# Kernel tuning notes

Hardware: AMD Instinct MI355X
Metric: run time of the kernel (lower is better)

Reference implementation:

```python
import jax, jax.numpy as jnp
import numpy as np

N = 50000      # nodes
E = 800000     # edges per sampled adjacency
F_IN = 128     # input features
H = 256        # hidden
C = 112        # classes (ogbn-proteins)
L = 8          # num_layers
EPS = 1e-5     # BatchNorm eps


def setup_inputs() -> dict:
    key = jax.random.key(0)
    ks = jax.random.split(key, 8)
    x = jax.random.normal(ks[0], (N, F_IN), dtype=jnp.float32)
    edge1 = jax.random.randint(ks[1], (2, E), 0, N)
    edge2 = jax.random.randint(ks[2], (2, E), 0, N)
    in_W = jax.random.normal(ks[3], (F_IN, H), dtype=jnp.float32) * 0.05
    in_b = jnp.zeros((H,), jnp.float32)
    convW = jax.random.normal(ks[4], (L, H, H), dtype=jnp.float32) * 0.05
    convB = jnp.zeros((L, H), jnp.float32)
    bn_gamma = jnp.ones((L, H), jnp.float32)
    bn_beta = jnp.zeros((L, H), jnp.float32)
    out_W = jax.random.normal(ks[5], (H, C), dtype=jnp.float32) * 0.05
    out_b = jnp.zeros((C,), jnp.float32)
    layer_w = jax.random.normal(ks[6], (L,), dtype=jnp.float32)
    return dict(x=x, edge1=edge1, edge2=edge2, in_W=in_W, in_b=in_b,
                convW=convW, convB=convB, bn_gamma=bn_gamma, bn_beta=bn_beta,
                out_W=out_W, out_b=out_b, layer_w=layer_w)


def _gcn_norm(edge_index):
    # GCNConv default: add self-loops, sym-normalize D^{-1/2} A_hat D^{-1/2}.
    loops = jnp.arange(N)
    row = jnp.concatenate([edge_index[0], loops])  # source
    col = jnp.concatenate([edge_index[1], loops])  # target
    deg = jax.ops.segment_sum(jnp.ones_like(row, jnp.float32), col, num_segments=N)
    dinv = jnp.where(deg > 0, jax.lax.rsqrt(deg), 0.0)
    return row, col, dinv[row] * dinv[col]


def reference(x, edge1, edge2, in_W, in_b, convW, convB, bn_gamma, bn_beta,
              out_W, out_b, layer_w):
    adj1 = _gcn_norm(edge1)
    adj2 = _gcn_norm(edge2)
    h = x @ in_W + in_b                                  # input_fc: [N, H]
    w = jax.nn.softmax(layer_w)                          # residual layer weights
    acc = jnp.zeros_like(h)
    for i in range(L):
        row, col, norm = adj1 if i < L // 2 else adj2
        t = h @ convW[i] + convB[i]                      # GCNConv linear
        msg = t[row] * norm[:, None]                     # gather + scale  [E+N, H]
        h = jax.ops.segment_sum(msg, col, num_segments=N)  # scatter-add SpMM
        mu = h.mean(axis=0)                              # BatchNorm1d (batch stats)
        var = h.var(axis=0)
        h = (h - mu) * jax.lax.rsqrt(var + EPS) * bn_gamma[i] + bn_beta[i]
        h = jax.nn.relu(h)                               # dropout is identity in eval
        acc = acc + w[i] * h                             # weighted residual sum
    out = acc @ out_W + out_b                            # out_fc: [N, C]
    return jax.nn.log_softmax(out, axis=1)
```

## Files before the change

### kernel.cpp

```cpp
#include <hip/hip_runtime.h>
#include <math.h>

#define NN 50000
#define HH 256
#define FIN 128
#define CC 112
#define LL 8
#define EE 800000
#define EPSB 1e-5f
#define NGRP 8
#define NPG (NN / NGRP)

typedef unsigned short u16;
typedef unsigned int u32;
typedef __attribute__((ext_vector_type(8))) short bf16x8;
typedef __attribute__((ext_vector_type(4))) float f32x4;

__device__ __forceinline__ u16 f2bf(float f) {
    u32 u = __float_as_uint(f);
    u32 r = (u + 0x7FFFu + ((u >> 16) & 1u)) >> 16;
    return (u16)r;
}
__device__ __forceinline__ float bflo(u32 u) { return __uint_as_float(u << 16); }
__device__ __forceinline__ float bfhi(u32 u) { return __uint_as_float(u & 0xFFFF0000u); }
__device__ __forceinline__ float bf1(u16 u) { return __uint_as_float(((u32)u) << 16); }

__device__ __forceinline__ void gload16(const u16* g, u16* l) {
    __builtin_amdgcn_global_load_lds(
        (const __attribute__((address_space(1))) void*)g,
        (__attribute__((address_space(3))) void*)l, 16, 0, 0);
}

__global__ __launch_bounds__(256) void k_fill2(const int* __restrict__ ed1,
                                               const int* __restrict__ ed2,
                                               int* __restrict__ cur,
                                               u16* __restrict__ src1p,
                                               u16* __restrict__ src2p) {
    const int g = blockIdx.x & 7;
    const int bg = blockIdx.x >> 3;
    const int nthr = (gridDim.x >> 3) * 256;
    const int tid = bg * 256 + threadIdx.x;
    const int lo = g * NPG;

    for (int e = tid; e < EE; e += nthr) {
        int c = ed1[e + EE];
        if ((u32)(c - lo) < (u32)NPG) {
            int pos = atomicAdd(&cur[c], 1);
            src1p[(c << 6) + pos] = (u16)ed1[e];
        }
    }
    for (int e = tid; e < EE; e += nthr) {
        int c = ed2[e + EE];
        if ((u32)(c - lo) < (u32)NPG) {
            int pos = atomicAdd(&cur[NN + c], 1);
            src2p[(c << 6) + pos] = (u16)ed2[e];
        }
    }
}

__global__ void k_dinv2(const int* __restrict__ deg, float* __restrict__ dinv1,
                        float* __restrict__ dinv2, int n) {
    int v = blockIdx.x * blockDim.x + threadIdx.x;
    if (v >= 2 * n) return;
    float* d = (v < n) ? dinv1 : dinv2;
    int vv = (v < n) ? v : v - n;
    d[vv] = rsqrtf((float)(deg[v] + 1));
}

__global__ void k_wt(const float* __restrict__ W, u16* __restrict__ Wt, int K, int N) {
    __shared__ u16 sm[32][33];
    const float* Wl = W + (size_t)blockIdx.z * K * N;
    u16* Wtl = Wt + (size_t)blockIdx.z * K * N;
    int k0 = blockIdx.y * 32, n0 = blockIdx.x * 32;
    int tx = threadIdx.x, ty = threadIdx.y;
#pragma unroll
    for (int r = 0; r < 32; r += 8)
        sm[ty + r][tx] = f2bf(Wl[(size_t)(k0 + ty + r) * N + n0 + tx]);
    __syncthreads();
#pragma unroll
    for (int r = 0; r < 32; r += 8)
        Wtl[(size_t)(n0 + ty + r) * K + k0 + tx] = sm[tx][ty + r];
}

__global__ void k_outwt(const float* __restrict__ outW, const float* __restrict__ outb,
                        u16* __restrict__ outWt, float* __restrict__ obb) {
    int idx = blockIdx.x * 256 + threadIdx.x;
    if (idx >= 128 * 256) return;
    int n = idx >> 8, k = idx & 255;
    float v = (n < CC) ? outW[(size_t)k * CC + n] : 0.f;
    outWt[(size_t)n * HH + k] = f2bf(v);
    if (idx < 128) obb[idx] = (idx < CC) ? outb[idx] : 0.f;
}

__global__ void k_xcast(const float* __restrict__ x, u16* __restrict__ xb, int n4) {
    int i = blockIdx.x * blockDim.x + threadIdx.x;
    if (i >= n4) return;
    float4 v = ((const float4*)x)[i];
    ushort4 o;
    o.x = f2bf(v.x); o.y = f2bf(v.y); o.z = f2bf(v.z); o.w = f2bf(v.w);
    *(ushort4*)(xb + ((size_t)i << 2)) = o;
}

template <bool F32OUT, bool SWIZ>
__global__ __launch_bounds__(256) void k_gemm_bf16(const u16* __restrict__ A,
                                                   const u16* __restrict__ Bt,
                                                   const float* __restrict__ bias,
                                                   const float* __restrict__ rowscale,
                                                   void* __restrict__ Cout,
                                                   int M, int Nc, int K) {
    int m0, n0;
    if (SWIZ) {
        int id = blockIdx.x;
        int g = id >> 4, r = id & 15;
        int m = g * 8 + (r & 7);
        if (m * 128 >= M) return;
        m0 = m * 128;
        n0 = (r >> 3) * 128;
    } else {
        m0 = blockIdx.x * 128;
        n0 = 0;
    }
    __shared__ u16 As[128 * 32];
    __shared__ u16 Bs[128 * 32];
    const int tid = threadIdx.x;
    const int w = tid >> 6, lane = tid & 63;
    const int wr = (w >> 1) * 64, wc = (w & 1) * 64;
    const int lm = lane & 15, lq = lane >> 4;

    f32x4 acc[4][4];
#pragma unroll
    for (int i = 0; i < 4; ++i)
#pragma unroll
        for (int j = 0; j < 4; ++j) acc[i][j] = (f32x4){0.f, 0.f, 0.f, 0.f};

    const int srow = w * 16 + (lane >> 2);
    const int scol = (lane & 3) * 8;

    for (int k0 = 0; k0 < K; k0 += 32) {
        int gm = m0 + srow;        if (gm >= M) gm = M - 1;
        gload16(A + (size_t)gm * K + k0 + scol, As + (size_t)(w * 64) * 8);
        int gm2 = m0 + 64 + srow;  if (gm2 >= M) gm2 = M - 1;
        gload16(A + (size_t)gm2 * K + k0 + scol, As + (size_t)(256 + w * 64) * 8);
        gload16(Bt + (size_t)(n0 + srow) * K + k0 + scol, Bs + (size_t)(w * 64) * 8);
        gload16(Bt + (size_t)(n0 + 64 + srow) * K + k0 + scol, Bs + (size_t)(256 + w * 64) * 8);
        __syncthreads();

        bf16x8 af[4], bfr[4];
#pragma unroll
        for (int i = 0; i < 4; ++i)
            af[i] = *(const bf16x8*)(As + (wr + i * 16 + lm) * 32 + lq * 8);
#pragma unroll
        for (int j = 0; j < 4; ++j)
            bfr[j] = *(const bf16x8*)(Bs + (wc + j * 16 + lm) * 32 + lq * 8);
#pragma unroll
        for (int i = 0; i < 4; ++i)
#pragma unroll
            for (int j = 0; j < 4; ++j)
                acc[i][j] = __builtin_amdgcn_mfma_f32_16x16x32_bf16(af[i], bfr[j], acc[i][j], 0, 0, 0);
        __syncthreads();
    }

#pragma unroll
    for (int j = 0; j < 4; ++j) {
        int gc = n0 + wc + j * 16 + lm;
        float bj = (gc < Nc) ? bias[gc] : 0.f;
#pragma unroll
        for (int i = 0; i < 4; ++i) {
#pragma unroll
            for (int r = 0; r < 4; ++r) {
                int gr = m0 + wr + i * 16 + lq * 4 + r;
                if (gr < M && gc < Nc) {
                    float rs = rowscale ? rowscale[gr] : 1.0f;
                    float val = (acc[i][j][r] + bj) * rs;
                    if (F32OUT)
                        ((float*)Cout)[(size_t)gr * Nc + gc] = val;
                    else
                        ((u16*)Cout)[(size_t)gr * Nc + gc] = f2bf(val);
                }
            }
        }
    }
}

__global__ __launch_bounds__(512) void k_spmm_bf16(const u16* __restrict__ t,
                                                   const int* __restrict__ deg,
                                                   const u16* __restrict__ srcp,
                                                   const float* __restrict__ dinv,
                                                   u16* __restrict__ hpre,
                                                   float* __restrict__ bns,
                                                   float* __restrict__ bnq) {
    __shared__ float lsum[8][HH];
    __shared__ float lsq[8][HH];
    int w = threadIdx.x >> 6;
    int lane = threadIdx.x & 63;
    int c = lane << 2;
    const u16* tp = t + c;
    float4 ssum = make_float4(0.f, 0.f, 0.f, 0.f);
    float4 ssq  = make_float4(0.f, 0.f, 0.f, 0.f);
    int vbase = (blockIdx.x * 8 + w) * 2;

    for (int i = 0; i < 2; ++i) {
        int v = vbase + i;
        const u16* src = srcp + (v << 6);
        float dv = dinv[v];
        uint2 a = *(const uint2*)(tp + (size_t)v * HH);
        float4 accv;
        accv.x = bflo(a.x); accv.y = bfhi(a.x);
        accv.z = bflo(a.y); accv.w = bfhi(a.y);
        int end = deg[v];
        int j = 0;
        for (; j + 8 <= end; j += 8) {
            uint4 sp = *(const uint4*)(src + j);
            int s0 = sp.x & 0xFFFF, s1 = sp.x >> 16;
            int s2 = sp.y & 0xFFFF, s3 = sp.y >> 16;
            int s4 = sp.z & 0xFFFF, s5 = sp.z >> 16;
            int s6 = sp.w & 0xFFFF, s7 = sp.w >> 16;
            uint2 b0 = *(const uint2*)(tp + (size_t)s0 * HH);
            uint2 b1 = *(const uint2*)(tp + (size_t)s1 * HH);
            uint2 b2 = *(const uint2*)(tp + (size_t)s2 * HH);
            uint2 b3 = *(const uint2*)(tp + (size_t)s3 * HH);
            uint2 b4 = *(const uint2*)(tp + (size_t)s4 * HH);
            uint2 b5 = *(const uint2*)(tp + (size_t)s5 * HH);
            uint2 b6 = *(const uint2*)(tp + (size_t)s6 * HH);
            uint2 b7 = *(const uint2*)(tp + (size_t)s7 * HH);
            accv.x += bflo(b0.x) + bflo(b1.x) + bflo(b2.x) + bflo(b3.x)
                    + bflo(b4.x) + bflo(b5.x) + bflo(b6.x) + bflo(b7.x);
            accv.y += bfhi(b0.x) + bfhi(b1.x) + bfhi(b2.x) + bfhi(b3.x)
                    + bfhi(b4.x) + bfhi(b5.x) + bfhi(b6.x) + bfhi(b7.x);
            accv.z += bflo(b0.y) + bflo(b1.y) + bflo(b2.y) + bflo(b3.y)
                    + bflo(b4.y) + bflo(b5.y) + bflo(b6.y) + bflo(b7.y);
            accv.w += bfhi(b0.y) + bfhi(b1.y) + bfhi(b2.y) + bfhi(b3.y)
                    + bfhi(b4.y) + bfhi(b5.y) + bfhi(b6.y) + bfhi(b7.y);
        }
        for (; j + 2 <= end; j += 2) {
            int s0 = src[j], s1 = src[j + 1];
            uint2 b0 = *(const uint2*)(tp + (size_t)s0 * HH);
            uint2 b1 = *(const uint2*)(tp + (size_t)s1 * HH);
            accv.x += bflo(b0.x) + bflo(b1.x);
            accv.y += bfhi(b0.x) + bfhi(b1.x);
            accv.z += bflo(b0.y) + bflo(b1.y);
            accv.w += bfhi(b0.y) + bfhi(b1.y);
        }
        if (j < end) {
            int s0 = src[j];
            uint2 b0 = *(const uint2*)(tp + (size_t)s0 * HH);
            accv.x += bflo(b0.x); accv.y += bfhi(b0.x);
            accv.z += bflo(b0.y); accv.w += bfhi(b0.y);
        }
        ushort4 o;
        o.x = f2bf(accv.x * dv); o.y = f2bf(accv.y * dv);
        o.z = f2bf(accv.z * dv); o.w = f2bf(accv.w * dv);
        *(ushort4*)(hpre + (size_t)v * HH + c) = o;

        float vx = bf1(o.x), vy = bf1(o.y), vz = bf1(o.z), vw = bf1(o.w);
        ssum.x += vx; ssum.y += vy; ssum.z += vz; ssum.w += vw;
        ssq.x = fmaf(vx, vx, ssq.x); ssq.y = fmaf(vy, vy, ssq.y);
        ssq.z = fmaf(vz, vz, ssq.z); ssq.w = fmaf(vw, vw, ssq.w);
    }

    lsum[w][c + 0] = ssum.x; lsum[w][c + 1] = ssum.y;
    lsum[w][c + 2] = ssum.z; lsum[w][c + 3] = ssum.w;
    lsq[w][c + 0] = ssq.x; lsq[w][c + 1] = ssq.y;
    lsq[w][c + 2] = ssq.z; lsq[w][c + 3] = ssq.w;
    __syncthreads();
    int tid = threadIdx.x;
    if (tid < HH) {
        float s = 0.f;
#pragma unroll
        for (int ww = 0; ww < 8; ++ww) s += lsum[ww][tid];
        atomicAdd(&bns[(blockIdx.x & 7) * HH + tid], s);
    } else {
        int tcol = tid - HH;
        float q = 0.f;
#pragma unroll
        for (int ww = 0; ww < 8; ++ww) q += lsq[ww][tcol];
        atomicAdd(&bnq[(blockIdx.x & 7) * HH + tcol], q);
    }
}

__global__ __launch_bounds__(256) void k_bnnorm(const u16* __restrict__ hpre,
                         u16* __restrict__ accb, u16* __restrict__ hb,
                         const float* __restrict__ bins,
                         const float* __restrict__ gamma, const float* __restrict__ beta,
                         const float* __restrict__ wArr, int layer) {
    __shared__ float sscale[HH], sshift[HH];
    const float invN = 1.0f / (float)NN;
    {
        int tcol = threadIdx.x;
        float m = 0.f, qq = 0.f;
#pragma unroll
        for (int b = 0; b < 8; ++b) {
            m += bins[b * HH + tcol];
            qq += bins[(8 + b) * HH + tcol];
        }
        m *= invN;
        float var = qq * invN - m * m;
        float sc = rsqrtf(var + EPSB) * gamma[tcol];
        sscale[tcol] = sc;
        sshift[tcol] = beta[tcol] - m * sc;
    }
    __syncthreads();
    int idx = blockIdx.x * blockDim.x + threadIdx.x;
    if (idx >= NN * (HH / 4)) return;
    int c = (idx & 63) << 2;
    float w = wArr[layer];
    ushort4 hv = ((const ushort4*)hpre)[idx];
    ushort4 av = ((const ushort4*)accb)[idx];
    u16* hp = &hv.x;
    u16* ap = &av.x;
    ushort4 oh, oa;
    u16* ohp = &oh.x;
    u16* oap = &oa.x;
#pragma unroll
    for (int k = 0; k < 4; ++k) {
        float v = fmaf(bf1(hp[k]), sscale[c + k], sshift[c + k]);
        v = fmaxf(v, 0.f);
        oap[k] = f2bf(fmaf(w, v, bf1(ap[k])));
        ohp[k] = f2bf(v);
    }
    ((ushort4*)accb)[idx] = oa;
    *(ushort4*)(hb + ((size_t)idx << 2)) = oh;
}

__global__ void k_softmaxw(const float* __restrict__ lw, float* __restrict__ wArr) {
    if (threadIdx.x == 0 && blockIdx.x == 0) {
        float m = -3.0e38f;
        for (int i = 0; i < LL; ++i) m = fmaxf(m, lw[i]);
        float e[LL]; float sum = 0.f;
        for (int i = 0; i < LL; ++i) { e[i] = expf(lw[i] - m); sum += e[i]; }
        for (int i = 0; i < LL; ++i) wArr[i] = e[i] / sum;
    }
}

__global__ __launch_bounds__(256) void k_logsoftmax(const float* __restrict__ z,
                                                    float* __restrict__ out) {
    int gt = blockIdx.x * blockDim.x + threadIdx.x;
    int v = gt >> 6;
    int lane = threadIdx.x & 63;
    if (v >= NN) return;
    const float* row = z + (size_t)v * CC;
    float v0 = row[lane];
    float v1 = (lane + 64 < CC) ? row[lane + 64] : -3.0e38f;
    float m = fmaxf(v0, v1);
#pragma unroll
    for (int d = 1; d < 64; d <<= 1) m = fmaxf(m, __shfl_xor(m, d, 64));
    float e = expf(v0 - m) + ((lane + 64 < CC) ? expf(v1 - m) : 0.f);
#pragma unroll
    for (int d = 1; d < 64; d <<= 1) e += __shfl_xor(e, d, 64);
    float lse = m + logf(e);
    out[(size_t)v * CC + lane] = v0 - lse;
    if (lane + 64 < CC) out[(size_t)v * CC + lane + 64] = v1 - lse;
}

extern "C" void kernel_launch(void* const* d_in, const int* in_sizes, int n_in,
                              void* d_out, int out_size, void* d_ws, size_t ws_size,
                              hipStream_t stream) {
    const float* x     = (const float*)d_in[0];
    const int*   e1    = (const int*)d_in[1];
    const int*   e2    = (const int*)d_in[2];
    const float* inW   = (const float*)d_in[3];
    const float* inb   = (const float*)d_in[4];
    const float* convW = (const float*)d_in[5];
    const float* convB = (const float*)d_in[6];
    const float* gamma = (const float*)d_in[7];
    const float* beta  = (const float*)d_in[8];
    const float* outW  = (const float*)d_in[9];
    const float* outb  = (const float*)d_in[10];
    const float* lw    = (const float*)d_in[11];

    char* ws = (char*)d_ws;
    size_t off = 0;
    auto alloc = [&](size_t bytes) -> void* {
        void* p = ws + off;
        off = (off + bytes + 255) & ~(size_t)255;
        return p;
    };
    u16*   hb    = (u16*)alloc((size_t)NN * HH * 2);
    u16*   tb    = (u16*)alloc((size_t)NN * HH * 2);
    u16*   hpre  = (u16*)alloc((size_t)NN * HH * 2);
    u16*   accb  = (u16*)alloc((size_t)NN * HH * 2);
    u16*   convWt= (u16*)alloc((size_t)LL * HH * HH * 2);
    u16*   inWt  = (u16*)alloc((size_t)HH * FIN * 2);
    u16*   outWt = (u16*)alloc((size_t)128 * HH * 2);
    float* obb   = (float*)alloc(128 * 4);
    float* dinv1 = (float*)alloc((size_t)NN * 4);
    float* dinv2 = (float*)alloc((size_t)NN * 4);
    u16*   src1p = (u16*)alloc((size_t)NN * 64 * 2);
    u16*   src2p = (u16*)alloc((size_t)NN * 64 * 2);
    int*   curz  = (int*)alloc((size_t)2 * NN * 4);
    float* bnsq  = (float*)alloc((size_t)LL * 16 * HH * 4);
    float* wArr  = (float*)alloc(64);
    u16*   xb    = tb;
    float* logits = (float*)hpre;

    int* cur1 = curz;

    hipMemsetAsync(curz, 0, (size_t)2 * NN * 4, stream);
    hipMemsetAsync(bnsq, 0, (size_t)LL * 16 * HH * 4, stream);
    hipMemsetAsync(accb, 0, (size_t)NN * HH * 2, stream);

    k_fill2<<<8 * 256, 256, 0, stream>>>(e1, e2, curz, src1p, src2p);
    k_dinv2<<<(2 * NN + 255) / 256, 256, 0, stream>>>(curz, dinv1, dinv2, NN);

    k_softmaxw<<<1, 64, 0, stream>>>(lw, wArr);

    {
        dim3 g(HH / 32, HH / 32, LL);
        dim3 b(32, 8);
        k_wt<<<g, b, 0, stream>>>(convW, convWt, HH, HH);
        dim3 g2(HH / 32, FIN / 32, 1);
        k_wt<<<g2, b, 0, stream>>>(inW, inWt, FIN, HH);
        k_outwt<<<128, 256, 0, stream>>>(outW, outb, outWt, obb);
    }
    k_xcast<<<(NN * FIN / 4 + 255) / 256, 256, 0, stream>>>(x, xb, NN * FIN / 4);

    const int MT = (NN + 127) / 128;
    const int GSW = ((MT + 7) / 8) * 16;
    k_gemm_bf16<false, true><<<GSW, 256, 0, stream>>>(xb, inWt, inb, nullptr, hb, NN, HH, FIN);

    const int SPB = NN / 16;
    const int ELB = (NN * (HH / 4) + 255) / 256;
    for (int i = 0; i < LL; ++i) {
        const int* dg = (i < LL / 2) ? cur1 : (curz + NN);
        const u16* sr = (i < LL / 2) ? src1p : src2p;
        const float* dv = (i < LL / 2) ? dinv1 : dinv2;
        float* bins = bnsq + (size_t)i * 16 * HH;
        k_gemm_bf16<false, true><<<GSW, 256, 0, stream>>>(hb, convWt + (size_t)i * HH * HH,
                                                          convB + (size_t)i * HH, dv, tb,
                                                          NN, HH, HH);
        k_spmm_bf16<<<SPB, 512, 0, stream>>>(tb, dg, sr, dv, hpre,
                                             bins, bins + 8 * HH);
        k_bnnorm<<<ELB, 256, 0, stream>>>(hpre, accb, hb, bins,
                                          gamma + (size_t)i * HH, beta + (size_t)i * HH,
                                          wArr, i);
    }

    k_gemm_bf16<true, false><<<MT, 256, 0, stream>>>(accb, outWt, obb, nullptr, logits,
                                                     NN, CC, HH);
    k_logsoftmax<<<NN / 4, 256, 0, stream>>>(logits, (float*)d_out);
}
```

Measured before the change: 1.187 ms.

## Store GEMM output in column slices and gather per slice in SpMM

The conv GEMM now writes its bf16 output as eight 32-column slices, each contiguous over nodes, and the SpMM kernel is rewritten so each block handles one slice for 128 nodes. Each slice is about 3.2 MB, so the intent is to make random row gathers hit L2/LLC better than gathers over full 512-byte rows. In exchange, each gather touches only 64 bytes per row, there are more blocks and edge-index reads are repeated once per slice. BatchNorm partial statistics are reduced per slice.

```diff
diff --git a/kernel.cpp b/kernel.cpp
--- a/kernel.cpp
+++ b/kernel.cpp
@@ -10,6 +10,8 @@
 #define EPSB 1e-5f
 #define NGRP 8
 #define NPG (NN / NGRP)
+#define SLW 32
+#define NSL (HH / SLW)
 
 typedef unsigned short u16;
 typedef unsigned int u32;
@@ -101,7 +103,7 @@
     *(ushort4*)(xb + ((size_t)i << 2)) = o;
 }
 
-template <bool F32OUT, bool SWIZ>
+template <bool F32OUT, bool SWIZ, bool SLICED>
 __global__ __launch_bounds__(256) void k_gemm_bf16(const u16* __restrict__ A,
                                                    const u16* __restrict__ Bt,
                                                    const float* __restrict__ bias,
@@ -174,6 +176,8 @@
                     float val = (acc[i][j][r] + bj) * rs;
                     if (F32OUT)
                         ((float*)Cout)[(size_t)gr * Nc + gc] = val;
+                    else if (SLICED)
+                        ((u16*)Cout)[((size_t)(gc >> 5) * M + gr) * SLW + (gc & 31)] = f2bf(val);
                     else
                         ((u16*)Cout)[(size_t)gr * Nc + gc] = f2bf(val);
                 }
@@ -182,99 +186,89 @@
     }
 }
 
-__global__ __launch_bounds__(512) void k_spmm_bf16(const u16* __restrict__ t,
-                                                   const int* __restrict__ deg,
-                                                   const u16* __restrict__ srcp,
-                                                   const float* __restrict__ dinv,
-                                                   u16* __restrict__ hpre,
-                                                   float* __restrict__ bns,
-                                                   float* __restrict__ bnq) {
-    __shared__ float lsum[8][HH];
-    __shared__ float lsq[8][HH];
-    int w = threadIdx.x >> 6;
-    int lane = threadIdx.x & 63;
-    int c = lane << 2;
-    const u16* tp = t + c;
-    float4 ssum = make_float4(0.f, 0.f, 0.f, 0.f);
-    float4 ssq  = make_float4(0.f, 0.f, 0.f, 0.f);
-    int vbase = (blockIdx.x * 8 + w) * 2;
-
-    for (int i = 0; i < 2; ++i) {
-        int v = vbase + i;
-        const u16* src = srcp + (v << 6);
-        float dv = dinv[v];
-        uint2 a = *(const uint2*)(tp + (size_t)v * HH);
-        float4 accv;
-        accv.x = bflo(a.x); accv.y = bfhi(a.x);
-        accv.z = bflo(a.y); accv.w = bfhi(a.y);
-        int end = deg[v];
-        int j = 0;
-        for (; j + 8 <= end; j += 8) {
-            uint4 sp = *(const uint4*)(src + j);
-            int s0 = sp.x & 0xFFFF, s1 = sp.x >> 16;
-            int s2 = sp.y & 0xFFFF, s3 = sp.y >> 16;
-            int s4 = sp.z & 0xFFFF, s5 = sp.z >> 16;
-            int s6 = sp.w & 0xFFFF, s7 = sp.w >> 16;
-            uint2 b0 = *(const uint2*)(tp + (size_t)s0 * HH);
-            uint2 b1 = *(const uint2*)(tp + (size_t)s1 * HH);
-            uint2 b2 = *(const uint2*)(tp + (size_t)s2 * HH);
-            uint2 b3 = *(const uint2*)(tp + (size_t)s3 * HH);
-            uint2 b4 = *(const uint2*)(tp + (size_t)s4 * HH);
-            uint2 b5 = *(const uint2*)(tp + (size_t)s5 * HH);
-            uint2 b6 = *(const uint2*)(tp + (size_t)s6 * HH);
-            uint2 b7 = *(const uint2*)(tp + (size_t)s7 * HH);
-            accv.x += bflo(b0.x) + bflo(b1.x) + bflo(b2.x) + bflo(b3.x)
-                    + bflo(b4.x) + bflo(b5.x) + bflo(b6.x) + bflo(b7.x);
-            accv.y += bfhi(b0.x) + bfhi(b1.x) + bfhi(b2.x) + bfhi(b3.x)
-                    + bfhi(b4.x) + bfhi(b5.x) + bfhi(b6.x) + bfhi(b7.x);
-            accv.z += bflo(b0.y) + bflo(b1.y) + bflo(b2.y) + bflo(b3.y)
-                    + bflo(b4.y) + bflo(b5.y) + bflo(b6.y) + bflo(b7.y);
-            accv.w += bfhi(b0.y) + bfhi(b1.y) + bfhi(b2.y) + bfhi(b3.y)
-                    + bfhi(b4.y) + bfhi(b5.y) + bfhi(b6.y) + bfhi(b7.y);
+__global__ __launch_bounds__(512) void k_spmm_sl(const u16* __restrict__ ts,
+                                                 const int* __restrict__ deg,
+                                                 const u16* __restrict__ srcp,
+                                                 const float* __restrict__ dinv,
+                                                 u16* __restrict__ hpre,
+                                                 float* __restrict__ bns,
+                                                 float* __restrict__ bnq) {
+    __shared__ float lsum[32][33];
+    __shared__ float lsq[32][33];
+    const int s = blockIdx.x & 7;
+    const int nb = blockIdx.x >> 3;
+    const int w = threadIdx.x >> 6;
+    const int lane = threadIdx.x & 63;
+    const int sub = lane >> 4;
+    const int li = lane & 15;
+    const u16* tsl = ts + (size_t)s * NN * SLW + li * 2;
+    float2 ssum = {0.f, 0.f};
+    float2 ssq  = {0.f, 0.f};
+
+#pragma unroll
+    for (int it = 0; it < 4; ++it) {
+        int v = nb * 128 + it * 32 + w * 4 + sub;
+        if (v < NN) {
+            const u16* src = srcp + ((size_t)v << 6);
+            float dv = dinv[v];
+            u32 a = *(const u32*)(tsl + (size_t)v * SLW);
+            float ax = bflo(a), ay = bfhi(a);
+            int end = deg[v];
+            int j = 0;
+            for (; j + 8 <= end; j += 8) {
+                uint4 sp = *(const uint4*)(src + j);
+                int s0 = sp.x & 0xFFFF, s1 = sp.x >> 16;
+                int s2 = sp.y & 0xFFFF, s3 = sp.y >> 16;
+                int s4 = sp.z & 0xFFFF, s5 = sp.z >> 16;
+                int s6 = sp.w & 0xFFFF, s7 = sp.w >> 16;
+                u32 b0 = *(const u32*)(tsl + (size_t)s0 * SLW);
+                u32 b1 = *(const u32*)(tsl + (size_t)s1 * SLW);
+                u32 b2 = *(const u32*)(tsl + (size_t)s2 * SLW);
+                u32 b3 = *(const u32*)(tsl + (size_t)s3 * SLW);
+                u32 b4 = *(const u32*)(tsl + (size_t)s4 * SLW);
+                u32 b5 = *(const u32*)(tsl + (size_t)s5 * SLW);
+                u32 b6 = *(const u32*)(tsl + (size_t)s6 * SLW);
+                u32 b7 = *(const u32*)(tsl + (size_t)s7 * SLW);
+                ax += bflo(b0) + bflo(b1) + bflo(b2) + bflo(b3)
+                    + bflo(b4) + bflo(b5) + bflo(b6) + bflo(b7);
+                ay += bfhi(b0) + bfhi(b1) + bfhi(b2) + bfhi(b3)
+                    + bfhi(b4) + bfhi(b5) + bfhi(b6) + bfhi(b7);
+            }
+            for (; j + 2 <= end; j += 2) {
+                int s0 = src[j], s1 = src[j + 1];
+                u32 b0 = *(const u32*)(tsl + (size_t)s0 * SLW);
+                u32 b1 = *(const u32*)(tsl + (size_t)s1 * SLW);
+                ax += bflo(b0) + bflo(b1);
+                ay += bfhi(b0) + bfhi(b1);
+            }
+            if (j < end) {
+                u32 b0 = *(const u32*)(tsl + (size_t)src[j] * SLW);
+                ax += bflo(b0); ay += bfhi(b0);
+            }
+            u16 ox = f2bf(ax * dv), oy = f2bf(ay * dv);
+            *(u32*)(hpre + (size_t)v * HH + s * SLW + li * 2) = ((u32)oy << 16) | (u32)ox;
+            float fx = bf1(ox), fy = bf1(oy);
+            ssum.x += fx; ssum.y += fy;
+            ssq.x = fmaf(fx, fx, ssq.x); ssq.y = fmaf(fy, fy, ssq.y);
         }
-        for (; j + 2 <= end; j += 2) {
-            int s0 = src[j], s1 = src[j + 1];
-            uint2 b0 = *(const uint2*)(tp + (size_t)s0 * HH);
-            uint2 b1 = *(const uint2*)(tp + (size_t)s1 * HH);
-            accv.x += bflo(b0.x) + bflo(b1.x);
-            accv.y += bfhi(b0.x) + bfhi(b1.x);
-            accv.z += bflo(b0.y) + bflo(b1.y);
-            accv.w += bfhi(b0.y) + bfhi(b1.y);
-        }
-        if (j < end) {
-            int s0 = src[j];
-            uint2 b0 = *(const uint2*)(tp + (size_t)s0 * HH);
-            accv.x += bflo(b0.x); accv.y += bfhi(b0.x);
-            accv.z += bflo(b0.y); accv.w += bfhi(b0.y);
-        }
-        ushort4 o;
-        o.x = f2bf(accv.x * dv); o.y = f2bf(accv.y * dv);
-        o.z = f2bf(accv.z * dv); o.w = f2bf(accv.w * dv);
-        *(ushort4*)(hpre + (size_t)v * HH + c) = o;
-
-        float vx = bf1(o.x), vy = bf1(o.y), vz = bf1(o.z), vw = bf1(o.w);
-        ssum.x += vx; ssum.y += vy; ssum.z += vz; ssum.w += vw;
-        ssq.x = fmaf(vx, vx, ssq.x); ssq.y = fmaf(vy, vy, ssq.y);
-        ssq.z = fmaf(vz, vz, ssq.z); ssq.w = fmaf(vw, vw, ssq.w);
-    }
-
-    lsum[w][c + 0] = ssum.x; lsum[w][c + 1] = ssum.y;
-    lsum[w][c + 2] = ssum.z; lsum[w][c + 3] = ssum.w;
-    lsq[w][c + 0] = ssq.x; lsq[w][c + 1] = ssq.y;
-    lsq[w][c + 2] = ssq.z; lsq[w][c + 3] = ssq.w;
+    }
+
+    int row = w * 4 + sub;
+    lsum[row][li * 2] = ssum.x; lsum[row][li * 2 + 1] = ssum.y;
+    lsq[row][li * 2] = ssq.x;   lsq[row][li * 2 + 1] = ssq.y;
     __syncthreads();
-    int tid = threadIdx.x;
-    if (tid < HH) {
-        float s = 0.f;
-#pragma unroll
-        for (int ww = 0; ww < 8; ++ww) s += lsum[ww][tid];
-        atomicAdd(&bns[(blockIdx.x & 7) * HH + tid], s);
-    } else {
-        int tcol = tid - HH;
-        float q = 0.f;
-#pragma unroll
-        for (int ww = 0; ww < 8; ++ww) q += lsq[ww][tcol];
-        atomicAdd(&bnq[(blockIdx.x & 7) * HH + tcol], q);
+    int t = threadIdx.x;
+    if (t < 32) {
+        float a = 0.f;
+#pragma unroll
+        for (int r = 0; r < 32; ++r) a += lsum[r][t];
+        atomicAdd(&bns[(nb & 7) * HH + s * SLW + t], a);
+    } else if (t < 64) {
+        int c = t - 32;
+        float a = 0.f;
+#pragma unroll
+        for (int r = 0; r < 32; ++r) a += lsq[r][c];
+        atomicAdd(&bnq[(nb & 7) * HH + s * SLW + c], a);
     }
 }
 
@@ -416,26 +410,27 @@
 
     const int MT = (NN + 127) / 128;
     const int GSW = ((MT + 7) / 8) * 16;
-    k_gemm_bf16<false, true><<<GSW, 256, 0, stream>>>(xb, inWt, inb, nullptr, hb, NN, HH, FIN);
-
-    const int SPB = NN / 16;
+    k_gemm_bf16<false, true, false><<<GSW, 256, 0, stream>>>(xb, inWt, inb, nullptr, hb,
+                                                             NN, HH, FIN);
+
+    const int SPB = ((NN + 127) / 128) * NSL;
     const int ELB = (NN * (HH / 4) + 255) / 256;
     for (int i = 0; i < LL; ++i) {
         const int* dg = (i < LL / 2) ? cur1 : (curz + NN);
         const u16* sr = (i < LL / 2) ? src1p : src2p;
         const float* dv = (i < LL / 2) ? dinv1 : dinv2;
         float* bins = bnsq + (size_t)i * 16 * HH;
-        k_gemm_bf16<false, true><<<GSW, 256, 0, stream>>>(hb, convWt + (size_t)i * HH * HH,
+        k_gemm_bf16<false, true, true><<<GSW, 256, 0, stream>>>(hb,
+                                                          convWt + (size_t)i * HH * HH,
                                                           convB + (size_t)i * HH, dv, tb,
                                                           NN, HH, HH);
-        k_spmm_bf16<<<SPB, 512, 0, stream>>>(tb, dg, sr, dv, hpre,
-                                             bins, bins + 8 * HH);
+        k_spmm_sl<<<SPB, 512, 0, stream>>>(tb, dg, sr, dv, hpre, bins, bins + 8 * HH);
         k_bnnorm<<<ELB, 256, 0, stream>>>(hpre, accb, hb, bins,
                                           gamma + (size_t)i * HH, beta + (size_t)i * HH,
                                           wArr, i);
     }
 
-    k_gemm_bf16<true, false><<<MT, 256, 0, stream>>>(accb, outWt, obb, nullptr, logits,
-                                                     NN, CC, HH);
+    k_gemm_bf16<true, false, false><<<MT, 256, 0, stream>>>(accb, outWt, obb, nullptr, logits,
+                                                            NN, CC, HH);
     k_logsoftmax<<<NN / 4, 256, 0, stream>>>(logits, (float*)d_out);
 }
```

Result: slower. 1.278 ms (+7.7%).
